# Kernel optimization log

Measured on AMD Instinct MI355X. Metric: run time of the kernel, lower is better.

Reference implementation:

```python
import jax, jax.numpy as jnp
import numpy as np

N = 50000      # nodes
E = 800000     # edges (avg degree 16)
IN = 16        # input feature dim
H = 512        # hidden dim
L = 3          # num conv layers
G = 256        # graphs per batch
EPS = 1e-5


def setup_inputs() -> dict:
    key = jax.random.key(0)
    ks = jax.random.split(key, 10)
    s = lambda d: 1.0 / np.sqrt(d)
    x = jax.random.normal(ks[0], (N, IN), jnp.float32)
    edge_index = jax.random.randint(ks[1], (2, E), 0, N, dtype=jnp.int64)
    batch = jnp.sort(jax.random.randint(ks[2], (N,), 0, G, dtype=jnp.int64))
    W_in = jax.random.normal(ks[3], (IN, H), jnp.float32) * s(IN)
    b_in = jnp.zeros((H,), jnp.float32)
    W_root = jax.random.normal(ks[4], (L, H, H), jnp.float32) * s(H)
    W_neigh = jax.random.normal(ks[5], (L, H, H), jnp.float32) * s(H)
    b_conv = jnp.zeros((L, H), jnp.float32)
    ln_gamma = jnp.ones((L, H), jnp.float32)
    ln_beta = jnp.zeros((L, H), jnp.float32)
    W_out = jax.random.normal(ks[6], (H, H), jnp.float32) * s(H)
    b_out = jnp.zeros((H,), jnp.float32)
    return {
        'x': x, 'edge_index': edge_index, 'batch': batch,
        'W_in': W_in, 'b_in': b_in,
        'W_root': W_root, 'W_neigh': W_neigh, 'b_conv': b_conv,
        'ln_gamma': ln_gamma, 'ln_beta': ln_beta,
        'W_out': W_out, 'b_out': b_out,
    }


def layer_norm(h, gamma, beta):
    mu = jnp.mean(h, axis=-1, keepdims=True)
    var = jnp.mean((h - mu) ** 2, axis=-1, keepdims=True)
    return (h - mu) * jax.lax.rsqrt(var + EPS) * gamma + beta


def reference(x, edge_index, batch, W_in, b_in, W_root, W_neigh, b_conv,
              ln_gamma, ln_beta, W_out, b_out):
    src, dst = edge_index[0], edge_index[1]
    h = x @ W_in + b_in                                  # [N, H]
    for l in range(L):
        # GraphConv: root transform + sum-aggregated neighbor transform
        agg = jax.ops.segment_sum(h[src], dst, num_segments=N)   # [N, H]
        h = h @ W_root[l] + agg @ W_neigh[l] + b_conv[l]
        h = jax.nn.relu(layer_norm(h, ln_gamma[l], ln_beta[l]))
        # dropout is identity in eval mode
    # mean pool per graph
    pooled = jax.ops.segment_sum(h, batch, num_segments=G)        # [G, H]
    counts = jax.ops.segment_sum(jnp.ones((N, 1), h.dtype), batch, num_segments=G)
    pooled = pooled / jnp.maximum(counts, 1.0)
    return pooled @ W_out + b_out
```

## Files before the change

### kernel.cpp

```cpp
#include <hip/hip_runtime.h>
#include <hip/hip_fp16.h>
#include <stdint.h>

#define N_NODES 50000
#define N_EDGES 800000
#define DIM_IN  16
#define H       512
#define GRAPHS  256
#define AK      1024
#define KT_STEPS 32

typedef __attribute__((ext_vector_type(8))) short short8;
typedef __attribute__((ext_vector_type(8))) _Float16 half8;
typedef __attribute__((ext_vector_type(4))) float f32x4;
typedef __attribute__((ext_vector_type(2))) float f32x2;
typedef __attribute__((ext_vector_type(4))) unsigned int u32x4;
typedef __attribute__((ext_vector_type(2))) unsigned int u32x2;

__device__ __forceinline__ unsigned short f2bf(float f) {
    unsigned int u = __float_as_uint(f);
    return (unsigned short)((u + 0x7fffu + ((u >> 16) & 1u)) >> 16);
}
__device__ __forceinline__ unsigned short f2h(float f) {
    __half h = __float2half(f);
    return *(unsigned short*)&h;
}

#define GLOAD_LDS16(g, l) __builtin_amdgcn_global_load_lds( \
    (const __attribute__((address_space(1))) void*)(g), \
    (__attribute__((address_space(3))) void*)(l), 16, 0, 0)

__global__ void k_count(const int* __restrict__ ei, int* __restrict__ deg) {
    int t = blockIdx.x * 256 + threadIdx.x;
    if (t < N_EDGES) atomicAdd(&deg[ei[N_EDGES + t]], 1);
}

__global__ void k_scan1(const int* __restrict__ deg, int* __restrict__ off, int* __restrict__ bsum) {
    __shared__ int ls[512];
    int t = threadIdx.x; int gi = blockIdx.x * 512 + t;
    ls[t] = (gi < N_NODES) ? deg[gi] : 0;
    __syncthreads();
    for (int o = 1; o < 512; o <<= 1) {
        int u = (t >= o) ? ls[t - o] : 0;
        __syncthreads();
        ls[t] += u;
        __syncthreads();
    }
    if (gi < N_NODES) off[gi] = (t == 0) ? 0 : ls[t - 1];
    if (t == 511) bsum[blockIdx.x] = ls[511];
}

__global__ void k_scan2(int* bsum) {
    __shared__ int ls[128];
    int t = threadIdx.x;
    ls[t] = (t < 98) ? bsum[t] : 0;
    __syncthreads();
    for (int o = 1; o < 128; o <<= 1) {
        int u = (t >= o) ? ls[t - o] : 0;
        __syncthreads();
        ls[t] += u;
        __syncthreads();
    }
    if (t < 98) bsum[t] = (t == 0) ? 0 : ls[t - 1];
}

__global__ void k_scan3(int* __restrict__ off, const int* __restrict__ bsum, int* __restrict__ cur) {
    int i = blockIdx.x * 256 + threadIdx.x;
    if (i < N_NODES) {
        int v = off[i] + bsum[i >> 9];
        off[i] = v; cur[i] = v;
    }
    if (i == 0) off[N_NODES] = N_EDGES;
}

__global__ void k_fill(const int* __restrict__ ei, int* __restrict__ cur, int* __restrict__ csr) {
    int t = blockIdx.x * 256 + threadIdx.x;
    if (t < N_EDGES) {
        int d = ei[N_EDGES + t];
        int p = atomicAdd(&cur[d], 1);
        csr[p] = ei[t];
    }
}

__global__ void k_gemm_in(const float* __restrict__ x, const float* __restrict__ Win,
                          const float* __restrict__ bin, unsigned short* A) {
    __shared__ float Wl[DIM_IN * H];
    __shared__ float xl[16 * DIM_IN];
    __shared__ float bl[H];
    int t = threadIdx.x;
    const float4* W4 = (const float4*)Win;
    float4* Wl4 = (float4*)Wl;
#pragma unroll
    for (int i = 0; i < 8; i++) Wl4[t + 256 * i] = W4[t + 256 * i];
    bl[t] = bin[t]; bl[t + 256] = bin[t + 256];
    int r0 = blockIdx.x * 16;
    {
        int r = t >> 4, k = t & 15;
        int row = r0 + r;
        xl[t] = (row < N_NODES) ? x[row * DIM_IN + k] : 0.f;
    }
    __syncthreads();
    int c0 = t * 2;
    for (int r = 0; r < 16; r++) {
        int row = r0 + r;
        if (row >= N_NODES) break;
        float a0 = bl[c0], a1 = bl[c0 + 1];
#pragma unroll
        for (int k = 0; k < 16; k++) {
            float xv = xl[r * 16 + k];
            a0 += xv * Wl[k * 512 + c0];
            a1 += xv * Wl[k * 512 + c0 + 1];
        }
        unsigned int pack = ((unsigned int)f2bf(a1) << 16) | (unsigned int)f2bf(a0);
        *(unsigned int*)&A[(size_t)row * AK + c0] = pack;
    }
}

__global__ void k_tofp8(const unsigned short* __restrict__ A, unsigned char* __restrict__ h8) {
    int i = blockIdx.x * 256 + threadIdx.x;
    if (i >= N_NODES * 64) return;
    int row = i >> 6, g = i & 63;
    u32x4 v = *(const u32x4*)&A[(size_t)row * AK + g * 8];
    float f[8];
#pragma unroll
    for (int j = 0; j < 4; j++) {
        f[2 * j]     = __uint_as_float(v[j] << 16);
        f[2 * j + 1] = __uint_as_float(v[j] & 0xffff0000u);
    }
    int w0 = __builtin_amdgcn_cvt_pk_fp8_f32(f[0], f[1], 0, false);
    w0 = __builtin_amdgcn_cvt_pk_fp8_f32(f[2], f[3], w0, true);
    int w1 = __builtin_amdgcn_cvt_pk_fp8_f32(f[4], f[5], 0, false);
    w1 = __builtin_amdgcn_cvt_pk_fp8_f32(f[6], f[7], w1, true);
    u32x2 o; o[0] = (unsigned int)w0; o[1] = (unsigned int)w1;
    *(u32x2*)&h8[(size_t)row * 512 + g * 8] = o;
}

__global__ void k_aggregate(const int* __restrict__ off, const int* __restrict__ csr,
                            const unsigned char* __restrict__ h8, unsigned short* A) {
    int w = threadIdx.x >> 6, lane = threadIdx.x & 63;
    int n = blockIdx.x * 4 + w;
    if (n >= N_NODES) return;
    int s = off[n], e = off[n + 1];
    float acc[8] = {0, 0, 0, 0, 0, 0, 0, 0};
    const unsigned char* Ab = h8 + (size_t)lane * 8;

#define ACC_FP8(vv) { \
    f32x2 p0 = __builtin_amdgcn_cvt_pk_f32_fp8((int)(vv)[0], false); \
    f32x2 p1 = __builtin_amdgcn_cvt_pk_f32_fp8((int)(vv)[0], true);  \
    f32x2 p2 = __builtin_amdgcn_cvt_pk_f32_fp8((int)(vv)[1], false); \
    f32x2 p3 = __builtin_amdgcn_cvt_pk_f32_fp8((int)(vv)[1], true);  \
    acc[0] += p0[0]; acc[1] += p0[1]; acc[2] += p1[0]; acc[3] += p1[1]; \
    acc[4] += p2[0]; acc[5] += p2[1]; acc[6] += p3[0]; acc[7] += p3[1]; }

    for (int base = s; base < e; base += 64) {
        int m = e - base; if (m > 64) m = 64;
        int idx = (lane < m) ? csr[base + lane] : 0;
        int g = 0;
        for (; g + 4 <= m; g += 4) {
            int sn0 = __shfl(idx, g);
            int sn1 = __shfl(idx, g + 1);
            int sn2 = __shfl(idx, g + 2);
            int sn3 = __shfl(idx, g + 3);
            u32x2 v0 = *(const u32x2*)(Ab + ((size_t)sn0 << 9));
            u32x2 v1 = *(const u32x2*)(Ab + ((size_t)sn1 << 9));
            u32x2 v2 = *(const u32x2*)(Ab + ((size_t)sn2 << 9));
            u32x2 v3 = *(const u32x2*)(Ab + ((size_t)sn3 << 9));
            ACC_FP8(v0); ACC_FP8(v1); ACC_FP8(v2); ACC_FP8(v3);
        }
        for (; g < m; g++) {
            int sn = __shfl(idx, g);
            u32x2 v = *(const u32x2*)(Ab + ((size_t)sn << 9));
            ACC_FP8(v);
        }
    }
#undef ACC_FP8
    u32x4 hv;
#pragma unroll
    for (int j = 0; j < 4; j++) {
        hv[j] = ((unsigned int)f2h(acc[2 * j + 1]) << 16) | (unsigned int)f2h(acc[2 * j]);
    }
    *(u32x4*)&A[(size_t)n * AK + 512 + lane * 8] = hv;
}

__global__ __launch_bounds__(512, 4)
void k_gemm_layer(unsigned short* A, const unsigned short* __restrict__ Bp,
                  const float* __restrict__ bias, const float* __restrict__ gamma,
                  const float* __restrict__ beta) {
    extern __shared__ __align__(16) char smem[];
    int t = threadIdx.x, w = t >> 6, lane = t & 63;
    int wr = w >> 1, wc = w & 1;
    int rblk = blockIdx.x * 64;

    f32x4 acc[16];
#pragma unroll
    for (int i = 0; i < 16; i++) acc[i] = (f32x4)(0.f);

    int rowSt = rblk + w * 16 + (lane & 15);
    if (rowSt >= N_NODES) rowSt = N_NODES - 1;
    const unsigned short* gAst = A + (size_t)rowSt * AK + (lane >> 4) * 8;
    const unsigned short* gB = Bp + (size_t)lane * 8;

    auto STAGE = [&](int kt, int buf) {
        char* base = smem + buf * 36864;
        const unsigned short* gBk = gB + (size_t)kt * 32 * 512;
#pragma unroll
        for (int i = 0; i < 4; i++) {
            int cf = w * 4 + i;
            GLOAD_LDS16(gBk + (size_t)cf * 512, base + cf * 1024);
        }
        if (w < 4) GLOAD_LDS16(gAst + kt * 32, base + 32768 + w * 1024);
    };

    STAGE(0, 0);
    __syncthreads();

    for (int kt = 0; kt < 16; kt++) {
        int cur = kt & 1;
        STAGE(kt + 1, cur ^ 1);
        char* base = smem + cur * 36864;
        short8 av = *(const short8*)(base + 32768 + wr * 1024 + lane * 16);
#pragma unroll
        for (int i = 0; i < 16; i++) {
            short8 bv = *(const short8*)(base + (wc * 16 + i) * 1024 + lane * 16);
            acc[i] = __builtin_amdgcn_mfma_f32_16x16x32_bf16(av, bv, acc[i], 0, 0, 0);
        }
        __syncthreads();
    }
    for (int kt = 16; kt < 32; kt++) {
        int cur = kt & 1;
        if (kt + 1 < 32) STAGE(kt + 1, cur ^ 1);
        char* base = smem + cur * 36864;
        half8 av = *(const half8*)(base + 32768 + wr * 1024 + lane * 16);
#pragma unroll
        for (int i = 0; i < 16; i++) {
            half8 bv = *(const half8*)(base + (wc * 16 + i) * 1024 + lane * 16);
            acc[i] = __builtin_amdgcn_mfma_f32_16x16x32_f16(av, bv, acc[i], 0, 0, 0);
        }
        __syncthreads();
    }

    int g = lane >> 4, cl = lane & 15;
    float s[4] = {0, 0, 0, 0}, q[4] = {0, 0, 0, 0};
#pragma unroll
    for (int i = 0; i < 16; i++) {
        int col = wc * 256 + i * 16 + cl;
        float b = bias[col];
        f32x4 a = acc[i];
#pragma unroll
        for (int r = 0; r < 4; r++) {
            float v = a[r] + b;
            a[r] = v;
            s[r] += v;
            q[r] += v * v;
        }
        acc[i] = a;
    }
#pragma unroll
    for (int m = 1; m < 16; m <<= 1) {
#pragma unroll
        for (int r = 0; r < 4; r++) {
            s[r] += __shfl_xor(s[r], m);
            q[r] += __shfl_xor(q[r], m);
        }
    }
    float* pbuf = (float*)smem;
    if (cl == 0) {
#pragma unroll
        for (int r = 0; r < 4; r++) {
            pbuf[((wr * 2 + wc) * 16) + g * 4 + r] = s[r];
            pbuf[256 + ((wr * 2 + wc) * 16) + g * 4 + r] = q[r];
        }
    }
    __syncthreads();
    float mean[4], rs[4];
#pragma unroll
    for (int r = 0; r < 4; r++) {
        float sf = pbuf[(wr * 2) * 16 + g * 4 + r] + pbuf[(wr * 2 + 1) * 16 + g * 4 + r];
        float qf = pbuf[256 + (wr * 2) * 16 + g * 4 + r] + pbuf[256 + (wr * 2 + 1) * 16 + g * 4 + r];
        mean[r] = sf * (1.f / 512.f);
        float var = qf * (1.f / 512.f) - mean[r] * mean[r];
        rs[r] = rsqrtf(var + 1e-5f);
    }
    int row0 = rblk + wr * 16 + g * 4;
    bool ok[4];
#pragma unroll
    for (int r = 0; r < 4; r++) ok[r] = (row0 + r) < N_NODES;
#pragma unroll
    for (int i = 0; i < 16; i++) {
        int col = wc * 256 + i * 16 + cl;
        float ga = gamma[col], be = beta[col];
        f32x4 a = acc[i];
#pragma unroll
        for (int r = 0; r < 4; r++) {
            float o = (a[r] - mean[r]) * rs[r] * ga + be;
            o = fmaxf(o, 0.f);
            if (ok[r]) A[(size_t)(row0 + r) * AK + col] = f2bf(o);
        }
    }
}

__global__ void k_pool(const unsigned short* __restrict__ A, const int* __restrict__ batch,
                       float* __restrict__ pooled) {
    __shared__ float part[4 * 512];
    __shared__ int se[2];
    int g = blockIdx.x, t = threadIdx.x, w = t >> 6, lane = t & 63;
    if (t == 0) {
        int lo = 0, hi = N_NODES;
        while (lo < hi) { int m = (lo + hi) >> 1; if (batch[m] < g) lo = m + 1; else hi = m; }
        se[0] = lo;
        int lo2 = lo; hi = N_NODES;
        while (lo2 < hi) { int m = (lo2 + hi) >> 1; if (batch[m] < g + 1) lo2 = m + 1; else hi = m; }
        se[1] = lo2;
    }
    __syncthreads();
    int s = se[0], e = se[1];
    float acc[8] = {0, 0, 0, 0, 0, 0, 0, 0};
    for (int row = s + w; row < e; row += 4) {
        u32x4 v = *(const u32x4*)&A[(size_t)row * AK + lane * 8];
#pragma unroll
        for (int j = 0; j < 4; j++) {
            unsigned int uu = v[j];
            acc[2 * j]     += __uint_as_float(uu << 16);
            acc[2 * j + 1] += __uint_as_float(uu & 0xffff0000u);
        }
    }
#pragma unroll
    for (int j = 0; j < 8; j++) part[w * 512 + j * 64 + lane] = acc[j];
    __syncthreads();
    float cnt = fmaxf((float)(e - s), 1.f);
    for (int sidx = t; sidx < 512; sidx += 256) {
        float v = part[sidx] + part[512 + sidx] + part[1024 + sidx] + part[1536 + sidx];
        int col = (sidx & 63) * 8 + (sidx >> 6);
        pooled[(size_t)g * 512 + col] = v / cnt;
    }
}

__global__ void k_out(const float* __restrict__ pooled, const float* __restrict__ Wout,
                      const float* __restrict__ bout, float* __restrict__ out) {
    __shared__ float pl[512];
    int g = blockIdx.x, t = threadIdx.x;
    pl[t] = pooled[(size_t)g * 512 + t];
    pl[t + 256] = pooled[(size_t)g * 512 + t + 256];
    __syncthreads();
    float a0 = bout[t], a1 = bout[t + 256];
#pragma unroll 4
    for (int k = 0; k < 512; k++) {
        float p = pl[k];
        a0 += p * Wout[(size_t)k * 512 + t];
        a1 += p * Wout[(size_t)k * 512 + t + 256];
    }
    out[(size_t)g * 512 + t] = a0;
    out[(size_t)g * 512 + t + 256] = a1;
}

__global__ void k_pack_b(const float* __restrict__ Wr, const float* __restrict__ Wn,
                         unsigned short* __restrict__ Bp) {
    int t = blockIdx.x * 256 + threadIdx.x;
    if (t >= 3 * KT_STEPS * 32 * 64) return;
    int lane = t & 63;
    int u = t >> 6;
    int cf = u & 31; u >>= 5;
    int kt = u % KT_STEPS;
    int l  = u / KT_STEPS;
    int col = cf * 16 + (lane & 15);
    int kr0 = (kt & 15) * 32 + (lane >> 4) * 8;
    bool isRoot = (kt < 16);
    const float* W = (isRoot ? Wr : Wn) + (size_t)l * H * H;
    unsigned int words[4];
#pragma unroll
    for (int p = 0; p < 4; p++) {
        float v0 = W[(size_t)(kr0 + 2 * p) * H + col];
        float v1 = W[(size_t)(kr0 + 2 * p + 1) * H + col];
        unsigned short b0 = isRoot ? f2bf(v0) : f2h(v0);
        unsigned short b1 = isRoot ? f2bf(v1) : f2h(v1);
        words[p] = ((unsigned int)b1 << 16) | (unsigned int)b0;
    }
    u32x4 v; v[0] = words[0]; v[1] = words[1]; v[2] = words[2]; v[3] = words[3];
    *(u32x4*)&Bp[(size_t)t * 8] = v;
}

extern "C" void kernel_launch(void* const* d_in, const int* in_sizes, int n_in,
                              void* d_out, int out_size, void* d_ws, size_t ws_size,
                              hipStream_t stream) {
    const float* x     = (const float*)d_in[0];
    const int*   ei    = (const int*)d_in[1];
    const int*   batch = (const int*)d_in[2];
    const float* Win   = (const float*)d_in[3];
    const float* bin   = (const float*)d_in[4];
    const float* Wr    = (const float*)d_in[5];
    const float* Wn    = (const float*)d_in[6];
    const float* bconv = (const float*)d_in[7];
    const float* gamma = (const float*)d_in[8];
    const float* beta  = (const float*)d_in[9];
    const float* Wout  = (const float*)d_in[10];
    const float* bout  = (const float*)d_in[11];
    float* out = (float*)d_out;

    char* p = (char*)d_ws;
    auto carve = [&](size_t bytes) { char* r = p; p += (bytes + 255) & ~(size_t)255; return r; };
    unsigned short* A  = (unsigned short*)carve((size_t)N_NODES * AK * 2);
    unsigned char*  h8 = (unsigned char*)carve((size_t)N_NODES * 512);
    unsigned short* Bp = (unsigned short*)carve((size_t)3 * KT_STEPS * 32 * 64 * 8 * 2);
    int* csr  = (int*)carve((size_t)N_EDGES * 4);
    int* deg  = (int*)carve((size_t)N_NODES * 4);
    int* off  = (int*)carve((size_t)(N_NODES + 1) * 4);
    int* cur  = (int*)carve((size_t)N_NODES * 4);
    int* bsum = (int*)carve(1024);
    float* pooled = (float*)carve((size_t)GRAPHS * H * 4);

    hipMemsetAsync(deg, 0, (size_t)N_NODES * 4, stream);
    k_count<<<(N_EDGES + 255) / 256, 256, 0, stream>>>(ei, deg);
    k_scan1<<<98, 512, 0, stream>>>(deg, off, bsum);
    k_scan2<<<1, 128, 0, stream>>>(bsum);
    k_scan3<<<(N_NODES + 255) / 256, 256, 0, stream>>>(off, bsum, cur);
    k_fill<<<(N_EDGES + 255) / 256, 256, 0, stream>>>(ei, cur, csr);
    k_gemm_in<<<(N_NODES + 15) / 16, 256, 0, stream>>>(x, Win, bin, A);
    k_tofp8<<<(N_NODES * 64 + 255) / 256, 256, 0, stream>>>(A, h8);
    k_pack_b<<<(3 * KT_STEPS * 32 * 64) / 256, 256, 0, stream>>>(Wr, Wn, Bp);
    for (int l = 0; l < 3; l++) {
        k_aggregate<<<(N_NODES + 3) / 4, 256, 0, stream>>>(off, csr, h8, A);
        k_gemm_layer<<<(N_NODES + 63) / 64, 512, 73728, stream>>>(
            A, Bp + (size_t)l * KT_STEPS * 32 * 64 * 8,
            bconv + (size_t)l * H, gamma + (size_t)l * H, beta + (size_t)l * H);
        if (l < 2)
            k_tofp8<<<(N_NODES * 64 + 255) / 256, 256, 0, stream>>>(A, h8);
    }
    k_pool<<<GRAPHS, 256, 0, stream>>>(A, batch, pooled);
    k_out<<<GRAPHS, 256, 0, stream>>>(pooled, Wout, bout, out);
}
```

Before: 650.3 us.

## Fuse FP8 feature conversion into producer kernels and tighten GEMM pipeline waits

Removes the standalone k_tofp8 passes. The fp8 copy of node features is now written directly by k_gemm_in and by the layer GEMM epilogue, gated by a flag on the last layer. This cuts two full re-reads of the bf16 activation matrix plus a kernel launch per layer. The GEMM main loop is also merged into one loop with explicit vmcnt waits and raw s_barrier/sched_barrier, so the next stage's loads can overlap the current MFMAs. The costs are byte-granular scattered fp8 stores in the epilogue and reliance on hand-counted vmcnt values that must match the load count per wave.

```diff
diff --git a/kernel.cpp b/kernel.cpp
--- a/kernel.cpp
+++ b/kernel.cpp
@@ -83,7 +83,8 @@
 }
 
 __global__ void k_gemm_in(const float* __restrict__ x, const float* __restrict__ Win,
-                          const float* __restrict__ bin, unsigned short* A) {
+                          const float* __restrict__ bin, unsigned short* A,
+                          unsigned char* __restrict__ h8) {
     __shared__ float Wl[DIM_IN * H];
     __shared__ float xl[16 * DIM_IN];
     __shared__ float bl[H];
@@ -113,26 +114,9 @@
         }
         unsigned int pack = ((unsigned int)f2bf(a1) << 16) | (unsigned int)f2bf(a0);
         *(unsigned int*)&A[(size_t)row * AK + c0] = pack;
-    }
-}
-
-__global__ void k_tofp8(const unsigned short* __restrict__ A, unsigned char* __restrict__ h8) {
-    int i = blockIdx.x * 256 + threadIdx.x;
-    if (i >= N_NODES * 64) return;
-    int row = i >> 6, g = i & 63;
-    u32x4 v = *(const u32x4*)&A[(size_t)row * AK + g * 8];
-    float f[8];
-#pragma unroll
-    for (int j = 0; j < 4; j++) {
-        f[2 * j]     = __uint_as_float(v[j] << 16);
-        f[2 * j + 1] = __uint_as_float(v[j] & 0xffff0000u);
-    }
-    int w0 = __builtin_amdgcn_cvt_pk_fp8_f32(f[0], f[1], 0, false);
-    w0 = __builtin_amdgcn_cvt_pk_fp8_f32(f[2], f[3], w0, true);
-    int w1 = __builtin_amdgcn_cvt_pk_fp8_f32(f[4], f[5], 0, false);
-    w1 = __builtin_amdgcn_cvt_pk_fp8_f32(f[6], f[7], w1, true);
-    u32x2 o; o[0] = (unsigned int)w0; o[1] = (unsigned int)w1;
-    *(u32x2*)&h8[(size_t)row * 512 + g * 8] = o;
+        unsigned int pk8 = (unsigned int)__builtin_amdgcn_cvt_pk_fp8_f32(a0, a1, 0, false);
+        *(unsigned short*)&h8[(size_t)row * 512 + c0] = (unsigned short)(pk8 & 0xffffu);
+    }
 }
 
 __global__ void k_aggregate(const int* __restrict__ off, const int* __restrict__ csr,
@@ -185,7 +169,8 @@
 __global__ __launch_bounds__(512, 4)
 void k_gemm_layer(unsigned short* A, const unsigned short* __restrict__ Bp,
                   const float* __restrict__ bias, const float* __restrict__ gamma,
-                  const float* __restrict__ beta) {
+                  const float* __restrict__ beta,
+                  unsigned char* __restrict__ h8, int w8) {
     extern __shared__ __align__(16) char smem[];
     int t = threadIdx.x, w = t >> 6, lane = t & 63;
     int wr = w >> 1, wc = w & 1;
@@ -212,31 +197,36 @@
     };
 
     STAGE(0, 0);
-    __syncthreads();
-
-    for (int kt = 0; kt < 16; kt++) {
+
+    for (int kt = 0; kt < KT_STEPS; kt++) {
         int cur = kt & 1;
-        STAGE(kt + 1, cur ^ 1);
+        if (kt + 1 < KT_STEPS) {
+            STAGE(kt + 1, cur ^ 1);
+            if (w < 4) asm volatile("s_waitcnt vmcnt(5)" ::: "memory");
+            else       asm volatile("s_waitcnt vmcnt(4)" ::: "memory");
+        } else {
+            asm volatile("s_waitcnt vmcnt(0)" ::: "memory");
+        }
+        __builtin_amdgcn_s_barrier();
+        __builtin_amdgcn_sched_barrier(0);
         char* base = smem + cur * 36864;
-        short8 av = *(const short8*)(base + 32768 + wr * 1024 + lane * 16);
-#pragma unroll
-        for (int i = 0; i < 16; i++) {
-            short8 bv = *(const short8*)(base + (wc * 16 + i) * 1024 + lane * 16);
-            acc[i] = __builtin_amdgcn_mfma_f32_16x16x32_bf16(av, bv, acc[i], 0, 0, 0);
-        }
-        __syncthreads();
-    }
-    for (int kt = 16; kt < 32; kt++) {
-        int cur = kt & 1;
-        if (kt + 1 < 32) STAGE(kt + 1, cur ^ 1);
-        char* base = smem + cur * 36864;
-        half8 av = *(const half8*)(base + 32768 + wr * 1024 + lane * 16);
-#pragma unroll
-        for (int i = 0; i < 16; i++) {
-            half8 bv = *(const half8*)(base + (wc * 16 + i) * 1024 + lane * 16);
-            acc[i] = __builtin_amdgcn_mfma_f32_16x16x32_f16(av, bv, acc[i], 0, 0, 0);
-        }
-        __syncthreads();
+        if (kt < 16) {
+            short8 av = *(const short8*)(base + 32768 + wr * 1024 + lane * 16);
+#pragma unroll
+            for (int i = 0; i < 16; i++) {
+                short8 bv = *(const short8*)(base + (wc * 16 + i) * 1024 + lane * 16);
+                acc[i] = __builtin_amdgcn_mfma_f32_16x16x32_bf16(av, bv, acc[i], 0, 0, 0);
+            }
+        } else {
+            half8 av = *(const half8*)(base + 32768 + wr * 1024 + lane * 16);
+#pragma unroll
+            for (int i = 0; i < 16; i++) {
+                half8 bv = *(const half8*)(base + (wc * 16 + i) * 1024 + lane * 16);
+                acc[i] = __builtin_amdgcn_mfma_f32_16x16x32_f16(av, bv, acc[i], 0, 0, 0);
+            }
+        }
+        __builtin_amdgcn_sched_barrier(0);
+        __builtin_amdgcn_s_barrier();
     }
 
     int g = lane >> 4, cl = lane & 15;
@@ -294,7 +284,13 @@
         for (int r = 0; r < 4; r++) {
             float o = (a[r] - mean[r]) * rs[r] * ga + be;
             o = fmaxf(o, 0.f);
-            if (ok[r]) A[(size_t)(row0 + r) * AK + col] = f2bf(o);
+            if (ok[r]) {
+                A[(size_t)(row0 + r) * AK + col] = f2bf(o);
+                if (w8) {
+                    unsigned int pk8 = (unsigned int)__builtin_amdgcn_cvt_pk_fp8_f32(o, o, 0, false);
+                    h8[(size_t)(row0 + r) * 512 + col] = (unsigned char)(pk8 & 0xffu);
+                }
+            }
         }
     }
 }
@@ -414,16 +410,14 @@
     k_scan2<<<1, 128, 0, stream>>>(bsum);
     k_scan3<<<(N_NODES + 255) / 256, 256, 0, stream>>>(off, bsum, cur);
     k_fill<<<(N_EDGES + 255) / 256, 256, 0, stream>>>(ei, cur, csr);
-    k_gemm_in<<<(N_NODES + 15) / 16, 256, 0, stream>>>(x, Win, bin, A);
-    k_tofp8<<<(N_NODES * 64 + 255) / 256, 256, 0, stream>>>(A, h8);
+    k_gemm_in<<<(N_NODES + 15) / 16, 256, 0, stream>>>(x, Win, bin, A, h8);
     k_pack_b<<<(3 * KT_STEPS * 32 * 64) / 256, 256, 0, stream>>>(Wr, Wn, Bp);
     for (int l = 0; l < 3; l++) {
         k_aggregate<<<(N_NODES + 3) / 4, 256, 0, stream>>>(off, csr, h8, A);
         k_gemm_layer<<<(N_NODES + 63) / 64, 512, 73728, stream>>>(
             A, Bp + (size_t)l * KT_STEPS * 32 * 64 * 8,
-            bconv + (size_t)l * H, gamma + (size_t)l * H, beta + (size_t)l * H);
-        if (l < 2)
-            k_tofp8<<<(N_NODES * 64 + 255) / 256, 256, 0, stream>>>(A, h8);
+            bconv + (size_t)l * H, gamma + (size_t)l * H, beta + (size_t)l * H,
+            h8, (l < 2) ? 1 : 0);
     }
     k_pool<<<GRAPHS, 256, 0, stream>>>(A, batch, pooled);
     k_out<<<GRAPHS, 256, 0, stream>>>(pooled, Wout, bout, out);
```

Measured after the change: 1.223 ms. 88.1% more time.

## Switch layer GEMM to 32x32x16 MFMA tiles and fuse fp8 conversion into input GEMM

Applied to the files above, without the earlier changes.

Rewrites the per-layer GEMM to use 32x32x16 bf16/f16 MFMA instructions, with a 2x4 wave grid where each wave owns 32 rows by 128 columns. The weight packing and the LayerNorm reduction/epilogue are reworked to match the new accumulator layout. The goal is fewer LDS reads per MFMA FLOP, since each A fragment is reused across more columns, and higher MFMA throughput per instruction. Separately, the input GEMM now writes the fp8 copy directly, which removes one k_tofp8 pass. The trade-offs are more shuffle and reduction work in the epilogue and a wider column stride in the output stores.

```diff
diff --git a/kernel.cpp b/kernel.cpp
--- a/kernel.cpp
+++ b/kernel.cpp
@@ -13,6 +13,7 @@
 typedef __attribute__((ext_vector_type(8))) short short8;
 typedef __attribute__((ext_vector_type(8))) _Float16 half8;
 typedef __attribute__((ext_vector_type(4))) float f32x4;
+typedef __attribute__((ext_vector_type(16))) float f32x16;
 typedef __attribute__((ext_vector_type(2))) float f32x2;
 typedef __attribute__((ext_vector_type(4))) unsigned int u32x4;
 typedef __attribute__((ext_vector_type(2))) unsigned int u32x2;
@@ -83,7 +84,8 @@
 }
 
 __global__ void k_gemm_in(const float* __restrict__ x, const float* __restrict__ Win,
-                          const float* __restrict__ bin, unsigned short* A) {
+                          const float* __restrict__ bin, unsigned short* A,
+                          unsigned char* __restrict__ h8) {
     __shared__ float Wl[DIM_IN * H];
     __shared__ float xl[16 * DIM_IN];
     __shared__ float bl[H];
@@ -113,6 +115,8 @@
         }
         unsigned int pack = ((unsigned int)f2bf(a1) << 16) | (unsigned int)f2bf(a0);
         *(unsigned int*)&A[(size_t)row * AK + c0] = pack;
+        unsigned int pk8 = (unsigned int)__builtin_amdgcn_cvt_pk_fp8_f32(a0, a1, 0, false);
+        *(unsigned short*)&h8[(size_t)row * 512 + c0] = (unsigned short)(pk8 & 0xffffu);
     }
 }
 
@@ -188,12 +192,14 @@
                   const float* __restrict__ beta) {
     extern __shared__ __align__(16) char smem[];
     int t = threadIdx.x, w = t >> 6, lane = t & 63;
-    int wr = w >> 1, wc = w & 1;
+    int wr = w >> 2, wc = w & 3;
     int rblk = blockIdx.x * 64;
-
-    f32x4 acc[16];
-#pragma unroll
-    for (int i = 0; i < 16; i++) acc[i] = (f32x4)(0.f);
+    int khalf = lane >> 5;
+    int rowhalf = (lane >> 4) & 1;
+
+    f32x16 acc4[4];
+#pragma unroll
+    for (int i = 0; i < 4; i++) acc4[i] = (f32x16)(0.f);
 
     int rowSt = rblk + w * 16 + (lane & 15);
     if (rowSt >= N_NODES) rowSt = N_NODES - 1;
@@ -205,24 +211,31 @@
         const unsigned short* gBk = gB + (size_t)kt * 32 * 512;
 #pragma unroll
         for (int i = 0; i < 4; i++) {
-            int cf = w * 4 + i;
-            GLOAD_LDS16(gBk + (size_t)cf * 512, base + cf * 1024);
+            int c = w * 4 + i;
+            GLOAD_LDS16(gBk + (size_t)c * 512, base + c * 1024);
         }
         if (w < 4) GLOAD_LDS16(gAst + kt * 32, base + 32768 + w * 1024);
     };
 
     STAGE(0, 0);
     __syncthreads();
+
+    int aoff = 32768 + (wr * 2 + rowhalf) * 1024 + (lane & 15) * 16 + khalf * 256;
+    int boff = lane * 16;
 
     for (int kt = 0; kt < 16; kt++) {
         int cur = kt & 1;
         STAGE(kt + 1, cur ^ 1);
         char* base = smem + cur * 36864;
-        short8 av = *(const short8*)(base + 32768 + wr * 1024 + lane * 16);
-#pragma unroll
-        for (int i = 0; i < 16; i++) {
-            short8 bv = *(const short8*)(base + (wc * 16 + i) * 1024 + lane * 16);
-            acc[i] = __builtin_amdgcn_mfma_f32_16x16x32_bf16(av, bv, acc[i], 0, 0, 0);
+        short8 av0 = *(const short8*)(base + aoff);
+        short8 av1 = *(const short8*)(base + aoff + 512);
+#pragma unroll
+        for (int cf = 0; cf < 4; cf++) {
+            int cfg = wc * 4 + cf;
+            short8 bv0 = *(const short8*)(base + cfg * 2048 + boff);
+            short8 bv1 = *(const short8*)(base + cfg * 2048 + 1024 + boff);
+            acc4[cf] = __builtin_amdgcn_mfma_f32_32x32x16_bf16(av0, bv0, acc4[cf], 0, 0, 0);
+            acc4[cf] = __builtin_amdgcn_mfma_f32_32x32x16_bf16(av1, bv1, acc4[cf], 0, 0, 0);
         }
         __syncthreads();
     }
@@ -230,35 +243,41 @@
         int cur = kt & 1;
         if (kt + 1 < 32) STAGE(kt + 1, cur ^ 1);
         char* base = smem + cur * 36864;
-        half8 av = *(const half8*)(base + 32768 + wr * 1024 + lane * 16);
-#pragma unroll
-        for (int i = 0; i < 16; i++) {
-            half8 bv = *(const half8*)(base + (wc * 16 + i) * 1024 + lane * 16);
-            acc[i] = __builtin_amdgcn_mfma_f32_16x16x32_f16(av, bv, acc[i], 0, 0, 0);
-        }
-        __syncthreads();
-    }
-
-    int g = lane >> 4, cl = lane & 15;
-    float s[4] = {0, 0, 0, 0}, q[4] = {0, 0, 0, 0};
-#pragma unroll
-    for (int i = 0; i < 16; i++) {
-        int col = wc * 256 + i * 16 + cl;
+        half8 av0 = *(const half8*)(base + aoff);
+        half8 av1 = *(const half8*)(base + aoff + 512);
+#pragma unroll
+        for (int cf = 0; cf < 4; cf++) {
+            int cfg = wc * 4 + cf;
+            half8 bv0 = *(const half8*)(base + cfg * 2048 + boff);
+            half8 bv1 = *(const half8*)(base + cfg * 2048 + 1024 + boff);
+            acc4[cf] = __builtin_amdgcn_mfma_f32_32x32x16_f16(av0, bv0, acc4[cf], 0, 0, 0);
+            acc4[cf] = __builtin_amdgcn_mfma_f32_32x32x16_f16(av1, bv1, acc4[cf], 0, 0, 0);
+        }
+        __syncthreads();
+    }
+
+    int cl = lane & 31;
+    float s[16], q[16];
+#pragma unroll
+    for (int r = 0; r < 16; r++) { s[r] = 0.f; q[r] = 0.f; }
+#pragma unroll
+    for (int cf = 0; cf < 4; cf++) {
+        int col = (wc * 4 + cf) * 32 + cl;
         float b = bias[col];
-        f32x4 a = acc[i];
-#pragma unroll
-        for (int r = 0; r < 4; r++) {
+        f32x16 a = acc4[cf];
+#pragma unroll
+        for (int r = 0; r < 16; r++) {
             float v = a[r] + b;
             a[r] = v;
             s[r] += v;
             q[r] += v * v;
         }
-        acc[i] = a;
-    }
-#pragma unroll
-    for (int m = 1; m < 16; m <<= 1) {
-#pragma unroll
-        for (int r = 0; r < 4; r++) {
+        acc4[cf] = a;
+    }
+#pragma unroll
+    for (int m = 1; m < 32; m <<= 1) {
+#pragma unroll
+        for (int r = 0; r < 16; r++) {
             s[r] += __shfl_xor(s[r], m);
             q[r] += __shfl_xor(q[r], m);
         }
@@ -266,35 +285,36 @@
     float* pbuf = (float*)smem;
     if (cl == 0) {
 #pragma unroll
-        for (int r = 0; r < 4; r++) {
-            pbuf[((wr * 2 + wc) * 16) + g * 4 + r] = s[r];
-            pbuf[256 + ((wr * 2 + wc) * 16) + g * 4 + r] = q[r];
-        }
-    }
-    __syncthreads();
-    float mean[4], rs[4];
-#pragma unroll
-    for (int r = 0; r < 4; r++) {
-        float sf = pbuf[(wr * 2) * 16 + g * 4 + r] + pbuf[(wr * 2 + 1) * 16 + g * 4 + r];
-        float qf = pbuf[256 + (wr * 2) * 16 + g * 4 + r] + pbuf[256 + (wr * 2 + 1) * 16 + g * 4 + r];
+        for (int r = 0; r < 16; r++) {
+            int rloc = (r & 3) + 8 * (r >> 2) + 4 * khalf;
+            pbuf[(wr * 32 + rloc) * 4 + wc] = s[r];
+            pbuf[256 + (wr * 32 + rloc) * 4 + wc] = q[r];
+        }
+    }
+    __syncthreads();
+    float mean[16], rs[16];
+#pragma unroll
+    for (int r = 0; r < 16; r++) {
+        int rloc = (r & 3) + 8 * (r >> 2) + 4 * khalf;
+        int bi = (wr * 32 + rloc) * 4;
+        float sf = pbuf[bi] + pbuf[bi + 1] + pbuf[bi + 2] + pbuf[bi + 3];
+        float qf = pbuf[256 + bi] + pbuf[256 + bi + 1] + pbuf[256 + bi + 2] + pbuf[256 + bi + 3];
         mean[r] = sf * (1.f / 512.f);
         float var = qf * (1.f / 512.f) - mean[r] * mean[r];
         rs[r] = rsqrtf(var + 1e-5f);
     }
-    int row0 = rblk + wr * 16 + g * 4;
-    bool ok[4];
-#pragma unroll
-    for (int r = 0; r < 4; r++) ok[r] = (row0 + r) < N_NODES;
-#pragma unroll
-    for (int i = 0; i < 16; i++) {
-        int col = wc * 256 + i * 16 + cl;
+#pragma unroll
+    for (int cf = 0; cf < 4; cf++) {
+        int col = (wc * 4 + cf) * 32 + cl;
         float ga = gamma[col], be = beta[col];
-        f32x4 a = acc[i];
-#pragma unroll
-        for (int r = 0; r < 4; r++) {
+        f32x16 a = acc4[cf];
+#pragma unroll
+        for (int r = 0; r < 16; r++) {
+            int rloc = (r & 3) + 8 * (r >> 2) + 4 * khalf;
+            int row = rblk + wr * 32 + rloc;
             float o = (a[r] - mean[r]) * rs[r] * ga + be;
             o = fmaxf(o, 0.f);
-            if (ok[r]) A[(size_t)(row0 + r) * AK + col] = f2bf(o);
+            if (row < N_NODES) A[(size_t)row * AK + col] = f2bf(o);
         }
     }
 }
@@ -359,11 +379,12 @@
     if (t >= 3 * KT_STEPS * 32 * 64) return;
     int lane = t & 63;
     int u = t >> 6;
-    int cf = u & 31; u >>= 5;
+    int c = u & 31; u >>= 5;
     int kt = u % KT_STEPS;
     int l  = u / KT_STEPS;
-    int col = cf * 16 + (lane & 15);
-    int kr0 = (kt & 15) * 32 + (lane >> 4) * 8;
+    int cf = c >> 1, sub = c & 1;
+    int col = cf * 32 + (lane & 31);
+    int kr0 = (kt & 15) * 32 + sub * 16 + (lane >> 5) * 8;
     bool isRoot = (kt < 16);
     const float* W = (isRoot ? Wr : Wn) + (size_t)l * H * H;
     unsigned int words[4];
@@ -414,8 +435,7 @@
     k_scan2<<<1, 128, 0, stream>>>(bsum);
     k_scan3<<<(N_NODES + 255) / 256, 256, 0, stream>>>(off, bsum, cur);
     k_fill<<<(N_EDGES + 255) / 256, 256, 0, stream>>>(ei, cur, csr);
-    k_gemm_in<<<(N_NODES + 15) / 16, 256, 0, stream>>>(x, Win, bin, A);
-    k_tofp8<<<(N_NODES * 64 + 255) / 256, 256, 0, stream>>>(A, h8);
+    k_gemm_in<<<(N_NODES + 15) / 16, 256, 0, stream>>>(x, Win, bin, A, h8);
     k_pack_b<<<(3 * KT_STEPS * 32 * 64) / 256, 256, 0, stream>>>(Wr, Wn, Bp);
     for (int l = 0; l < 3; l++) {
         k_aggregate<<<(N_NODES + 3) / 4, 256, 0, stream>>>(off, csr, h8, A);
```

Measured after the change: 773.9 us. 19.0% more time.
